# Optimization experiments

Measured on AMD Instinct MI355X. Metric: run time of the kernel, lower is better.

The kernel has to match this reference:

```python
import jax, jax.numpy as jnp
import numpy as np

B = 32768      # batch of ODE state evaluations
N = 64         # input_size (number of variables / per-node MLPs)
H = 64         # hidden_size
N_DISCRETE = 16  # first 16 variables use straight-through gating
HIDDEN_FLAG = True


def setup_inputs() -> dict:
    key = jax.random.key(0)
    k1, k2, k3 = jax.random.split(key, 3)
    inputs = jax.random.normal(k1, (B, N), jnp.float32)
    # Stacked per-node MLP weights: net_i is Linear(N,H,bias=False) -> ReLU -> Linear(H,1,bias=False)
    W1 = jax.random.normal(k2, (N, H, N), jnp.float32) / np.sqrt(N).astype(np.float32)
    W2 = jax.random.normal(k3, (N, H), jnp.float32) / np.sqrt(H).astype(np.float32)
    adjacency = jnp.ones((N, N), jnp.float32)  # buffer, initialized to ones
    discrete_mask = jnp.arange(N) < N_DISCRETE  # bool [N], from input_type_list
    return {"t": 0, "inputs": inputs, "W1": W1, "W2": W2,
            "adjacency": adjacency, "discrete_mask": discrete_mask}


def reference(t, inputs, W1, W2, adjacency, discrete_mask):
    # Straight-through discrete gating: y_hard - sg(y_soft) + y_soft
    y_soft = jax.nn.sigmoid(inputs)
    st = (inputs > 0).astype(inputs.dtype) - jax.lax.stop_gradient(y_soft) + y_soft
    x = jnp.where(discrete_mask[None, :], st, inputs)  # [B, N]

    # Effective per-node input mask: row i of adjacency; last node additionally
    # filtered to only its own (hidden) feature when hidden_flag is set.
    M = adjacency
    if HIDDEN_FLAG:
        one_hot_last = jnp.zeros((N,), M.dtype).at[-1].set(1.0)
        M = M.at[-1].set(M[-1] * one_hot_last)

    # Masking the input of node i by M[i] is equivalent to masking W1[i]'s input dim.
    W1m = W1 * M[:, None, :]                      # [N, H, N]
    h = jax.nn.relu(jnp.einsum('bn,ihn->bih', x, W1m))  # [B, N, H]
    out = jnp.einsum('bih,ih->bi', h, W2)               # [B, N]
    return out
```

## Files before the change

### kernel.cpp

```cpp
#include <hip/hip_runtime.h>
#include <stdint.h>


typedef __attribute__((ext_vector_type(8))) short short8;
typedef __attribute__((ext_vector_type(4))) float floatx4;

#define NN 64
#define HH 64
#define BB 32768
#define OTW 17
#define X_ELEMS (BB * NN)
#define W1_ELEMS (NN * HH * NN)

__device__ __forceinline__ unsigned short f32_to_bf16_bits(float f) {
    union { float f; unsigned int i; } c; c.f = f;
    unsigned int b = c.i;
    b += 0x7fffu + ((b >> 16) & 1u);
    return (unsigned short)(b >> 16);
}

__device__ __forceinline__ bool sniff_bf16(const void* x) {
    const int lane = threadIdx.x & 63;
    const ushort* xw = (const ushort*)x;
    const ushort a = xw[4 * lane];
    const ushort b = xw[4 * lane + 2];
    const int ea = (a >> 7) & 0xFF, eb = (b >> 7) & 0xFF;
    const int hit = ((ea >= 118 && ea <= 132) ? 1 : 0) + ((eb >= 118 && eb <= 132) ? 1 : 0);
    const unsigned long long m1 = __ballot(hit >= 1);
    const unsigned long long m2 = __ballot(hit >= 2);
    return (__popcll(m1) + __popcll(m2)) >= 64;
}

__global__ __launch_bounds__(256, 4)
void prep_kernel(const void* __restrict__ x, const void* __restrict__ w1,
                 ushort* __restrict__ xo, ushort* __restrict__ w1o)
{
    const bool is_bf16 = sniff_bf16(x);
    const long base = ((long)blockIdx.x * 256 + (long)threadIdx.x) * 8;

    if (base < X_ELEMS) {
        const bool gate = (base & 63) < 16;
        short8 v;
        if (is_bf16) {
            v = *(const short8*)((const ushort*)x + base);
            if (gate) {
                #pragma unroll
                for (int j = 0; j < 8; ++j) {
                    const unsigned short u = (unsigned short)v[j];
                    const bool pos = ((u & 0x8000u) == 0) && ((u & 0x7fffu) != 0);
                    v[j] = pos ? (short)0x3F80 : (short)0;
                }
            }
        } else {
            const float* p = (const float*)x + base;
            const float4 f0 = *(const float4*)(p);
            const float4 f1 = *(const float4*)(p + 4);
            const float vals[8] = {f0.x, f0.y, f0.z, f0.w, f1.x, f1.y, f1.z, f1.w};
            #pragma unroll
            for (int j = 0; j < 8; ++j) {
                if (gate) v[j] = (vals[j] > 0.f) ? (short)0x3F80 : (short)0;
                else      v[j] = (short)f32_to_bf16_bits(vals[j]);
            }
        }
        *(short8*)(xo + base) = v;
    } else {
        const long wb = base - X_ELEMS;
        if (wb < W1_ELEMS) {
            short8 v;
            if (is_bf16) {
                v = *(const short8*)((const ushort*)w1 + wb);
            } else {
                const float* p = (const float*)w1 + wb;
                const float4 f0 = *(const float4*)(p);
                const float4 f1 = *(const float4*)(p + 4);
                const float vals[8] = {f0.x, f0.y, f0.z, f0.w, f1.x, f1.y, f1.z, f1.w};
                #pragma unroll
                for (int j = 0; j < 8; ++j) v[j] = (short)f32_to_bf16_bits(vals[j]);
            }
            const int node = (int)(wb >> 12);
            if (node == NN - 1) {
                const int w63 = (int)(wb & 63);
                #pragma unroll
                for (int j = 0; j < 8; ++j)
                    if (w63 + j != NN - 1) v[j] = 0;
            }
            *(short8*)(w1o + wb) = v;
        }
    }
}

template<bool F32>
__device__ __forceinline__ void main_body(const ushort* __restrict__ xo,
                                          const ushort* __restrict__ w1o,
                                          const void* __restrict__ w2p,
                                          void* __restrict__ outp,
                                          float* outTile)
{
    const int tid  = threadIdx.x;
    const int wave = tid >> 6;
    const int lane = tid & 63;
    const int quad = lane >> 4;
    const int l16  = lane & 15;

    const int blk  = blockIdx.x;
    const int ng   = blk >> 9;
    const int rbg  = blk & 511;
    const int b0   = rbg * 64;
    const int nbase = ng * 16 + wave * 4;

    short8 xfrag[2][4];
    #pragma unroll
    for (int ks = 0; ks < 2; ++ks)
        #pragma unroll
        for (int nt = 0; nt < 4; ++nt)
            xfrag[ks][nt] = *(const short8*)(xo + (b0 + nt * 16 + l16) * NN + ks * 32 + quad * 8);

    short8 wcur[2][4], wnxt[2][4];
    {
        const ushort* w1n = w1o + nbase * (HH * NN);
        #pragma unroll
        for (int ks = 0; ks < 2; ++ks)
            #pragma unroll
            for (int mt = 0; mt < 4; ++mt)
                wcur[ks][mt] = *(const short8*)(w1n + (mt * 16 + l16) * NN + ks * 32 + quad * 8);
    }

    #pragma unroll 1
    for (int nl = 0; nl < 4; ++nl) {
        const int node = nbase + nl;

        if (nl < 3) {
            const ushort* w1n = w1o + (node + 1) * (HH * NN);
            #pragma unroll
            for (int ks = 0; ks < 2; ++ks)
                #pragma unroll
                for (int mt = 0; mt < 4; ++mt)
                    wnxt[ks][mt] = *(const short8*)(w1n + (mt * 16 + l16) * NN + ks * 32 + quad * 8);
        }

        float w2v[4][4];
        #pragma unroll
        for (int mt = 0; mt < 4; ++mt) {
            const int idx = node * HH + mt * 16 + quad * 4;
            if (F32) {
                const float4 w = *(const float4*)((const float*)w2p + idx);
                w2v[mt][0] = w.x; w2v[mt][1] = w.y; w2v[mt][2] = w.z; w2v[mt][3] = w.w;
            } else {
                const ushort4 w = *(const ushort4*)((const ushort*)w2p + idx);
                union { unsigned int i; float f; } c0, c1, c2, c3;
                c0.i = ((unsigned int)w.x) << 16; c1.i = ((unsigned int)w.y) << 16;
                c2.i = ((unsigned int)w.z) << 16; c3.i = ((unsigned int)w.w) << 16;
                w2v[mt][0] = c0.f; w2v[mt][1] = c1.f; w2v[mt][2] = c2.f; w2v[mt][3] = c3.f;
            }
        }

        floatx4 acc[4][4];
        #pragma unroll
        for (int mt = 0; mt < 4; ++mt)
            #pragma unroll
            for (int nt = 0; nt < 4; ++nt)
                acc[mt][nt] = (floatx4){0.f, 0.f, 0.f, 0.f};

        #pragma unroll
        for (int ks = 0; ks < 2; ++ks)
            #pragma unroll
            for (int mt = 0; mt < 4; ++mt)
                #pragma unroll
                for (int nt = 0; nt < 4; ++nt)
                    acc[mt][nt] = __builtin_amdgcn_mfma_f32_16x16x32_bf16(
                        wcur[ks][mt], xfrag[ks][nt], acc[mt][nt], 0, 0, 0);

        float psum[4];
        #pragma unroll
        for (int nt = 0; nt < 4; ++nt) {
            float s0 = 0.f, s1 = 0.f;
            #pragma unroll
            for (int mt = 0; mt < 4; ++mt) {
                float a0 = acc[mt][nt][0]; a0 = a0 > 0.f ? a0 : 0.f;
                float a1 = acc[mt][nt][1]; a1 = a1 > 0.f ? a1 : 0.f;
                float a2 = acc[mt][nt][2]; a2 = a2 > 0.f ? a2 : 0.f;
                float a3 = acc[mt][nt][3]; a3 = a3 > 0.f ? a3 : 0.f;
                s0 = fmaf(a0, w2v[mt][0], s0); s1 = fmaf(a1, w2v[mt][1], s1);
                s0 = fmaf(a2, w2v[mt][2], s0); s1 = fmaf(a3, w2v[mt][3], s1);
            }
            psum[nt] = s0 + s1;
        }

        #pragma unroll
        for (int nt = 0; nt < 4; ++nt) {
            psum[nt] += __shfl_xor(psum[nt], 16, 64);
            psum[nt] += __shfl_xor(psum[nt], 32, 64);
        }

        const float val = (quad == 0) ? psum[0] : (quad == 1) ? psum[1]
                         : (quad == 2) ? psum[2] : psum[3];
        outTile[lane * OTW + wave * 4 + nl] = val;

        if (nl < 3) {
            #pragma unroll
            for (int ks = 0; ks < 2; ++ks)
                #pragma unroll
                for (int mt = 0; mt < 4; ++mt)
                    wcur[ks][mt] = wnxt[ks][mt];
        }
    }

    __syncthreads();

    const int row = tid >> 2;
    const int c   = tid & 3;
    const float* rp = outTile + row * OTW + c * 4;
    const float4 v = make_float4(rp[0], rp[1], rp[2], rp[3]);
    const size_t obase = (size_t)(b0 + row) * NN + ng * 16 + c * 4;
    if (F32) {
        *(float4*)((float*)outp + obase) = v;
    } else {
        ushort4 o;
        o.x = f32_to_bf16_bits(v.x); o.y = f32_to_bf16_bits(v.y);
        o.z = f32_to_bf16_bits(v.z); o.w = f32_to_bf16_bits(v.w);
        *(ushort4*)((ushort*)outp + obase) = o;
    }
}

__global__ __launch_bounds__(256, 2)
void main_kernel(const void* __restrict__ xorig,
                 const ushort* __restrict__ xo, const ushort* __restrict__ w1o,
                 const void* __restrict__ w2p, void* __restrict__ outp)
{
    __shared__ float outTile[64 * OTW];
    const bool is_bf16 = sniff_bf16(xorig);
    if (is_bf16) main_body<false>(xo, w1o, w2p, outp, outTile);
    else         main_body<true >(xo, w1o, w2p, outp, outTile);
}

#define LDSW 20
template<bool F32>
__device__ __forceinline__ void run_body_fb(const void* xp, const void* w1p,
                                            const void* w2p, void* outp,
                                            float* myLds)
{
    const int tid  = threadIdx.x;
    const int wave = tid >> 6;
    const int lane = tid & 63;
    const int quad = lane >> 4;
    const int l16  = lane & 15;
    const int blk  = blockIdx.x;
    const int ng   = blk >> 7;
    const int rbg  = blk & 127;
    const int node = ng * 4 + wave;
    const int rowbase = rbg * 256;

    short8 bfrag[2][4];
    #pragma unroll
    for (int ks = 0; ks < 2; ++ks) {
        #pragma unroll
        for (int ht = 0; ht < 4; ++ht) {
            const int h = ht * 16 + l16;
            const int k = ks * 32 + quad * 8;
            short8 v;
            if (F32) {
                const float* p = (const float*)w1p + node * (HH * NN) + h * NN + k;
                const float4 a0 = *(const float4*)(p);
                const float4 a1 = *(const float4*)(p + 4);
                const float vals[8] = {a0.x, a0.y, a0.z, a0.w, a1.x, a1.y, a1.z, a1.w};
                #pragma unroll
                for (int j = 0; j < 8; ++j) v[j] = (short)f32_to_bf16_bits(vals[j]);
            } else {
                v = *(const short8*)((const ushort*)w1p + node * (HH * NN) + h * NN + k);
            }
            if (node == NN - 1) {
                #pragma unroll
                for (int j = 0; j < 8; ++j)
                    if (k + j != NN - 1) v[j] = 0;
            }
            bfrag[ks][ht] = v;
        }
    }

    float w2reg[4];
    #pragma unroll
    for (int ht = 0; ht < 4; ++ht) {
        const int idx = node * HH + ht * 16 + l16;
        if (F32) {
            w2reg[ht] = ((const float*)w2p)[idx];
        } else {
            const ushort u = ((const ushort*)w2p)[idx];
            union { unsigned int i; float f; } cv; cv.i = ((unsigned int)u) << 16;
            w2reg[ht] = cv.f;
        }
    }

    #pragma unroll 1
    for (int it = 0; it < 4; ++it) {
        const int b0 = rowbase + it * 64;
        short8 afrag[2][4];
        #pragma unroll
        for (int ks = 0; ks < 2; ++ks) {
            #pragma unroll
            for (int rt = 0; rt < 4; ++rt) {
                const int rowg = b0 + rt * 16 + l16;
                const int k    = ks * 32 + quad * 8;
                const bool gate = (ks == 0 && quad < 2);
                short8 v;
                if (F32) {
                    const float* p = (const float*)xp + rowg * NN + k;
                    const float4 a0 = *(const float4*)(p);
                    const float4 a1 = *(const float4*)(p + 4);
                    const float vals[8] = {a0.x, a0.y, a0.z, a0.w, a1.x, a1.y, a1.z, a1.w};
                    #pragma unroll
                    for (int j = 0; j < 8; ++j) {
                        if (gate) v[j] = (vals[j] > 0.f) ? (short)0x3F80 : (short)0;
                        else      v[j] = (short)f32_to_bf16_bits(vals[j]);
                    }
                } else {
                    v = *(const short8*)((const ushort*)xp + rowg * NN + k);
                    if (gate) {
                        #pragma unroll
                        for (int j = 0; j < 8; ++j) {
                            const unsigned short u = (unsigned short)v[j];
                            const bool pos = ((u & 0x8000u) == 0) && ((u & 0x7fffu) != 0);
                            v[j] = pos ? (short)0x3F80 : (short)0;
                        }
                    }
                }
                afrag[ks][rt] = v;
            }
        }

        floatx4 acc[4][4];
        #pragma unroll
        for (int rt = 0; rt < 4; ++rt)
            #pragma unroll
            for (int ht = 0; ht < 4; ++ht)
                acc[rt][ht] = (floatx4){0.f, 0.f, 0.f, 0.f};
        #pragma unroll
        for (int ks = 0; ks < 2; ++ks)
            #pragma unroll
            for (int rt = 0; rt < 4; ++rt)
                #pragma unroll
                for (int ht = 0; ht < 4; ++ht)
                    acc[rt][ht] = __builtin_amdgcn_mfma_f32_16x16x32_bf16(
                        afrag[ks][rt], bfrag[ks][ht], acc[rt][ht], 0, 0, 0);

        #pragma unroll
        for (int rt = 0; rt < 4; ++rt) {
            #pragma unroll
            for (int r = 0; r < 4; ++r) {
                float s = 0.f;
                #pragma unroll
                for (int ht = 0; ht < 4; ++ht) {
                    float v = acc[rt][ht][r];
                    v = v > 0.f ? v : 0.f;
                    s = fmaf(v, w2reg[ht], s);
                }
                myLds[(rt * 16 + quad * 4 + r) * LDSW + l16] = s;
            }
        }
        __syncthreads();
        const float* rowp = myLds + lane * LDSW;
        const float4 v0 = *(const float4*)(rowp + 0);
        const float4 v1 = *(const float4*)(rowp + 4);
        const float4 v2 = *(const float4*)(rowp + 8);
        const float4 v3 = *(const float4*)(rowp + 12);
        const float tot = (((v0.x + v0.y) + (v0.z + v0.w)) + ((v1.x + v1.y) + (v1.z + v1.w)))
                        + (((v2.x + v2.y) + (v2.z + v2.w)) + ((v3.x + v3.y) + (v3.z + v3.w)));
        if (F32) ((float*) outp)[(size_t)(b0 + lane) * NN + node] = tot;
        else     ((ushort*)outp)[(size_t)(b0 + lane) * NN + node] = f32_to_bf16_bits(tot);
        __syncthreads();
    }
}

__global__ __launch_bounds__(256, 2)
void fallback_kernel(const void* __restrict__ x, const void* __restrict__ W1,
                     const void* __restrict__ W2, void* __restrict__ out)
{
    __shared__ float lds[4][64 * LDSW];
    const bool is_bf16 = sniff_bf16(x);
    float* myLds = &lds[threadIdx.x >> 6][0];
    if (is_bf16) run_body_fb<false>(x, W1, W2, out, myLds);
    else         run_body_fb<true >(x, W1, W2, out, myLds);
}

extern "C" void kernel_launch(void* const* d_in, const int* in_sizes, int n_in,
                              void* d_out, int out_size, void* d_ws, size_t ws_size,
                              hipStream_t stream) {
    int i_in = -1, i_w1 = -1, i_w2 = -1;
    for (int i = 0; i < n_in; ++i) {
        const int s = in_sizes[i];
        if      (s == BB * NN  && i_in < 0) i_in = i;
        else if (s == NN*HH*NN && i_w1 < 0) i_w1 = i;
        else if (s == NN*HH    && i_w2 < 0) i_w2 = i;
    }
    if (i_in < 0) i_in = (n_in > 1) ? 1 : 0;
    if (i_w1 < 0) i_w1 = i_in + 1;
    if (i_w2 < 0) i_w2 = i_w1 + 1;

    const size_t need = (size_t)(X_ELEMS + W1_ELEMS) * sizeof(ushort);
    if (ws_size >= need) {
        ushort* xo  = (ushort*)d_ws;
        ushort* w1o = xo + X_ELEMS;
        prep_kernel<<<dim3((X_ELEMS + W1_ELEMS) / (256 * 8)), dim3(256), 0, stream>>>(
            d_in[i_in], d_in[i_w1], xo, w1o);
        main_kernel<<<dim3(4 * 512), dim3(256), 0, stream>>>(
            d_in[i_in], xo, w1o, d_in[i_w2], d_out);
    } else {
        fallback_kernel<<<dim3(16 * 128), dim3(256), 0, stream>>>(
            d_in[i_in], d_in[i_w1], d_in[i_w2], d_out);
    }
}
```

Measured before the change: 118.7 us.

## Process all 64 nodes per block to reuse x fragments across nodes

Each block now covers a 64-row batch tile across all 64 nodes, with every wave handling 16 nodes, instead of 16 nodes per block in a grid four times larger. This loads each x tile once instead of four times and writes full 64-wide output rows. W1 double-buffering changes to a ping-pong scheme with two register sets, and the output tile in shared memory widens to 64 columns. The cost is a grid of only 512 blocks, which may underfill the GPU's CUs, plus longer per-block serial work and the same W1 traffic spread over fewer blocks.

```diff
diff --git a/kernel.cpp b/kernel.cpp
--- a/kernel.cpp
+++ b/kernel.cpp
@@ -8,7 +8,7 @@
 #define NN 64
 #define HH 64
 #define BB 32768
-#define OTW 17
+#define OTW 65
 #define X_ELEMS (BB * NN)
 #define W1_ELEMS (NN * HH * NN)
 
@@ -102,11 +102,9 @@
     const int quad = lane >> 4;
     const int l16  = lane & 15;
 
-    const int blk  = blockIdx.x;
-    const int ng   = blk >> 9;
-    const int rbg  = blk & 511;
-    const int b0   = rbg * 64;
-    const int nbase = ng * 16 + wave * 4;
+    const int blk = blockIdx.x;
+    const int b0  = blk * 64;
+    const int nbase = wave * 16;
 
     short8 xfrag[2][4];
     #pragma unroll
@@ -115,41 +113,28 @@
         for (int nt = 0; nt < 4; ++nt)
             xfrag[ks][nt] = *(const short8*)(xo + (b0 + nt * 16 + l16) * NN + ks * 32 + quad * 8);
 
-    short8 wcur[2][4], wnxt[2][4];
-    {
-        const ushort* w1n = w1o + nbase * (HH * NN);
+    auto loadW1 = [&](short8 w[2][4], int node) {
+        const ushort* w1n = w1o + node * (HH * NN);
         #pragma unroll
         for (int ks = 0; ks < 2; ++ks)
             #pragma unroll
             for (int mt = 0; mt < 4; ++mt)
-                wcur[ks][mt] = *(const short8*)(w1n + (mt * 16 + l16) * NN + ks * 32 + quad * 8);
-    }
-
-    #pragma unroll 1
-    for (int nl = 0; nl < 4; ++nl) {
-        const int node = nbase + nl;
-
-        if (nl < 3) {
-            const ushort* w1n = w1o + (node + 1) * (HH * NN);
-            #pragma unroll
-            for (int ks = 0; ks < 2; ++ks)
-                #pragma unroll
-                for (int mt = 0; mt < 4; ++mt)
-                    wnxt[ks][mt] = *(const short8*)(w1n + (mt * 16 + l16) * NN + ks * 32 + quad * 8);
-        }
-
+                w[ks][mt] = *(const short8*)(w1n + (mt * 16 + l16) * NN + ks * 32 + quad * 8);
+    };
+
+    auto computeNode = [&](const short8 w[2][4], int node) {
         float w2v[4][4];
         #pragma unroll
         for (int mt = 0; mt < 4; ++mt) {
             const int idx = node * HH + mt * 16 + quad * 4;
             if (F32) {
-                const float4 w = *(const float4*)((const float*)w2p + idx);
-                w2v[mt][0] = w.x; w2v[mt][1] = w.y; w2v[mt][2] = w.z; w2v[mt][3] = w.w;
+                const float4 ww = *(const float4*)((const float*)w2p + idx);
+                w2v[mt][0] = ww.x; w2v[mt][1] = ww.y; w2v[mt][2] = ww.z; w2v[mt][3] = ww.w;
             } else {
-                const ushort4 w = *(const ushort4*)((const ushort*)w2p + idx);
+                const ushort4 ww = *(const ushort4*)((const ushort*)w2p + idx);
                 union { unsigned int i; float f; } c0, c1, c2, c3;
-                c0.i = ((unsigned int)w.x) << 16; c1.i = ((unsigned int)w.y) << 16;
-                c2.i = ((unsigned int)w.z) << 16; c3.i = ((unsigned int)w.w) << 16;
+                c0.i = ((unsigned int)ww.x) << 16; c1.i = ((unsigned int)ww.y) << 16;
+                c2.i = ((unsigned int)ww.z) << 16; c3.i = ((unsigned int)ww.w) << 16;
                 w2v[mt][0] = c0.f; w2v[mt][1] = c1.f; w2v[mt][2] = c2.f; w2v[mt][3] = c3.f;
             }
         }
@@ -168,7 +153,7 @@
                 #pragma unroll
                 for (int nt = 0; nt < 4; ++nt)
                     acc[mt][nt] = __builtin_amdgcn_mfma_f32_16x16x32_bf16(
-                        wcur[ks][mt], xfrag[ks][nt], acc[mt][nt], 0, 0, 0);
+                        w[ks][mt], xfrag[ks][nt], acc[mt][nt], 0, 0, 0);
 
         float psum[4];
         #pragma unroll
@@ -194,31 +179,41 @@
 
         const float val = (quad == 0) ? psum[0] : (quad == 1) ? psum[1]
                          : (quad == 2) ? psum[2] : psum[3];
-        outTile[lane * OTW + wave * 4 + nl] = val;
-
-        if (nl < 3) {
-            #pragma unroll
-            for (int ks = 0; ks < 2; ++ks)
-                #pragma unroll
-                for (int mt = 0; mt < 4; ++mt)
-                    wcur[ks][mt] = wnxt[ks][mt];
-        }
+        outTile[lane * OTW + node] = val;
+    };
+
+    short8 wA[2][4], wB[2][4];
+    loadW1(wA, nbase);
+    #pragma unroll 1
+    for (int np = 0; np < 16; np += 2) {
+        loadW1(wB, nbase + np + 1);
+        computeNode(wA, nbase + np);
+        if (np + 2 < 16) loadW1(wA, nbase + np + 2);
+        computeNode(wB, nbase + np + 1);
     }
 
     __syncthreads();
 
     const int row = tid >> 2;
-    const int c   = tid & 3;
-    const float* rp = outTile + row * OTW + c * 4;
-    const float4 v = make_float4(rp[0], rp[1], rp[2], rp[3]);
-    const size_t obase = (size_t)(b0 + row) * NN + ng * 16 + c * 4;
+    const int q   = tid & 3;
+    const float* rp = outTile + row * OTW + q * 16;
+    const size_t obase = (size_t)(b0 + row) * NN + q * 16;
     if (F32) {
-        *(float4*)((float*)outp + obase) = v;
+        float* op = (float*)outp + obase;
+        #pragma unroll
+        for (int c = 0; c < 4; ++c) {
+            const float4 v = make_float4(rp[c*4+0], rp[c*4+1], rp[c*4+2], rp[c*4+3]);
+            *(float4*)(op + c * 4) = v;
+        }
     } else {
-        ushort4 o;
-        o.x = f32_to_bf16_bits(v.x); o.y = f32_to_bf16_bits(v.y);
-        o.z = f32_to_bf16_bits(v.z); o.w = f32_to_bf16_bits(v.w);
-        *(ushort4*)((ushort*)outp + obase) = o;
+        ushort* op = (ushort*)outp + obase;
+        #pragma unroll
+        for (int c = 0; c < 4; ++c) {
+            ushort4 o;
+            o.x = f32_to_bf16_bits(rp[c*4+0]); o.y = f32_to_bf16_bits(rp[c*4+1]);
+            o.z = f32_to_bf16_bits(rp[c*4+2]); o.w = f32_to_bf16_bits(rp[c*4+3]);
+            *(ushort4*)(op + c * 4) = o;
+        }
     }
 }
 
@@ -401,7 +396,7 @@
         ushort* w1o = xo + X_ELEMS;
         prep_kernel<<<dim3((X_ELEMS + W1_ELEMS) / (256 * 8)), dim3(256), 0, stream>>>(
             d_in[i_in], d_in[i_w1], xo, w1o);
-        main_kernel<<<dim3(4 * 512), dim3(256), 0, stream>>>(
+        main_kernel<<<dim3(512), dim3(256), 0, stream>>>(
             d_in[i_in], xo, w1o, d_in[i_w2], d_out);
     } else {
         fallback_kernel<<<dim3(16 * 128), dim3(256), 0, stream>>>(
```

New measurement: 115.1 us. -3.0%, faster.

## Retile main kernel to 32 rows by 32 nodes per block with single weight buffer

Applied to the files above, without the earlier changes.

Each block now covers 32 batch rows and 32 nodes (8 nodes per wave) instead of 64 rows and 16 nodes. The double-buffered weight registers become one buffer, with the next node's W1 load issued right after the MFMAs. Launch bounds rise to 3 blocks per SM. The aim is lower register pressure and higher occupancy. The cost is that each W1 fragment is reused over half as many batch rows, so per-wave arithmetic intensity drops and W1 is reloaded more often.

```diff
diff --git a/kernel.cpp b/kernel.cpp
--- a/kernel.cpp
+++ b/kernel.cpp
@@ -8,7 +8,7 @@
 #define NN 64
 #define HH 64
 #define BB 32768
-#define OTW 17
+#define OTW 33
 #define X_ELEMS (BB * NN)
 #define W1_ELEMS (NN * HH * NN)
 
@@ -102,63 +102,54 @@
     const int quad = lane >> 4;
     const int l16  = lane & 15;
 
-    const int blk  = blockIdx.x;
-    const int ng   = blk >> 9;
-    const int rbg  = blk & 511;
-    const int b0   = rbg * 64;
-    const int nbase = ng * 16 + wave * 4;
-
-    short8 xfrag[2][4];
+    const int blk    = blockIdx.x;
+    const int ngrp   = blk >> 10;
+    const int rchunk = blk & 1023;
+    const int b0     = rchunk * 32;
+    const int nbase  = ngrp * 32 + wave * 8;
+
+    short8 xfrag[2][2];
     #pragma unroll
     for (int ks = 0; ks < 2; ++ks)
         #pragma unroll
-        for (int nt = 0; nt < 4; ++nt)
+        for (int nt = 0; nt < 2; ++nt)
             xfrag[ks][nt] = *(const short8*)(xo + (b0 + nt * 16 + l16) * NN + ks * 32 + quad * 8);
 
-    short8 wcur[2][4], wnxt[2][4];
+    short8 w[2][4];
     {
         const ushort* w1n = w1o + nbase * (HH * NN);
         #pragma unroll
         for (int ks = 0; ks < 2; ++ks)
             #pragma unroll
             for (int mt = 0; mt < 4; ++mt)
-                wcur[ks][mt] = *(const short8*)(w1n + (mt * 16 + l16) * NN + ks * 32 + quad * 8);
+                w[ks][mt] = *(const short8*)(w1n + (mt * 16 + l16) * NN + ks * 32 + quad * 8);
     }
 
     #pragma unroll 1
-    for (int nl = 0; nl < 4; ++nl) {
+    for (int nl = 0; nl < 8; ++nl) {
         const int node = nbase + nl;
-
-        if (nl < 3) {
-            const ushort* w1n = w1o + (node + 1) * (HH * NN);
-            #pragma unroll
-            for (int ks = 0; ks < 2; ++ks)
-                #pragma unroll
-                for (int mt = 0; mt < 4; ++mt)
-                    wnxt[ks][mt] = *(const short8*)(w1n + (mt * 16 + l16) * NN + ks * 32 + quad * 8);
-        }
 
         float w2v[4][4];
         #pragma unroll
         for (int mt = 0; mt < 4; ++mt) {
             const int idx = node * HH + mt * 16 + quad * 4;
             if (F32) {
-                const float4 w = *(const float4*)((const float*)w2p + idx);
-                w2v[mt][0] = w.x; w2v[mt][1] = w.y; w2v[mt][2] = w.z; w2v[mt][3] = w.w;
+                const float4 ww = *(const float4*)((const float*)w2p + idx);
+                w2v[mt][0] = ww.x; w2v[mt][1] = ww.y; w2v[mt][2] = ww.z; w2v[mt][3] = ww.w;
             } else {
-                const ushort4 w = *(const ushort4*)((const ushort*)w2p + idx);
+                const ushort4 ww = *(const ushort4*)((const ushort*)w2p + idx);
                 union { unsigned int i; float f; } c0, c1, c2, c3;
-                c0.i = ((unsigned int)w.x) << 16; c1.i = ((unsigned int)w.y) << 16;
-                c2.i = ((unsigned int)w.z) << 16; c3.i = ((unsigned int)w.w) << 16;
+                c0.i = ((unsigned int)ww.x) << 16; c1.i = ((unsigned int)ww.y) << 16;
+                c2.i = ((unsigned int)ww.z) << 16; c3.i = ((unsigned int)ww.w) << 16;
                 w2v[mt][0] = c0.f; w2v[mt][1] = c1.f; w2v[mt][2] = c2.f; w2v[mt][3] = c3.f;
             }
         }
 
-        floatx4 acc[4][4];
+        floatx4 acc[4][2];
         #pragma unroll
         for (int mt = 0; mt < 4; ++mt)
             #pragma unroll
-            for (int nt = 0; nt < 4; ++nt)
+            for (int nt = 0; nt < 2; ++nt)
                 acc[mt][nt] = (floatx4){0.f, 0.f, 0.f, 0.f};
 
         #pragma unroll
@@ -166,13 +157,22 @@
             #pragma unroll
             for (int mt = 0; mt < 4; ++mt)
                 #pragma unroll
-                for (int nt = 0; nt < 4; ++nt)
+                for (int nt = 0; nt < 2; ++nt)
                     acc[mt][nt] = __builtin_amdgcn_mfma_f32_16x16x32_bf16(
-                        wcur[ks][mt], xfrag[ks][nt], acc[mt][nt], 0, 0, 0);
-
-        float psum[4];
-        #pragma unroll
-        for (int nt = 0; nt < 4; ++nt) {
+                        w[ks][mt], xfrag[ks][nt], acc[mt][nt], 0, 0, 0);
+
+        if (nl < 7) {
+            const ushort* w1n = w1o + (node + 1) * (HH * NN);
+            #pragma unroll
+            for (int ks = 0; ks < 2; ++ks)
+                #pragma unroll
+                for (int mt = 0; mt < 4; ++mt)
+                    w[ks][mt] = *(const short8*)(w1n + (mt * 16 + l16) * NN + ks * 32 + quad * 8);
+        }
+
+        float psum[2];
+        #pragma unroll
+        for (int nt = 0; nt < 2; ++nt) {
             float s0 = 0.f, s1 = 0.f;
             #pragma unroll
             for (int mt = 0; mt < 4; ++mt) {
@@ -187,47 +187,40 @@
         }
 
         #pragma unroll
-        for (int nt = 0; nt < 4; ++nt) {
+        for (int nt = 0; nt < 2; ++nt) {
             psum[nt] += __shfl_xor(psum[nt], 16, 64);
             psum[nt] += __shfl_xor(psum[nt], 32, 64);
         }
 
-        const float val = (quad == 0) ? psum[0] : (quad == 1) ? psum[1]
-                         : (quad == 2) ? psum[2] : psum[3];
-        outTile[lane * OTW + wave * 4 + nl] = val;
-
-        if (nl < 3) {
-            #pragma unroll
-            for (int ks = 0; ks < 2; ++ks)
-                #pragma unroll
-                for (int mt = 0; mt < 4; ++mt)
-                    wcur[ks][mt] = wnxt[ks][mt];
-        }
+        const int half = lane >> 5;
+        const float val = half ? psum[1] : psum[0];
+        if ((lane & 16) == 0)
+            outTile[(half * 16 + l16) * OTW + wave * 8 + nl] = val;
     }
 
     __syncthreads();
 
-    const int row = tid >> 2;
-    const int c   = tid & 3;
+    const int row = tid >> 3;
+    const int c   = tid & 7;
     const float* rp = outTile + row * OTW + c * 4;
-    const float4 v = make_float4(rp[0], rp[1], rp[2], rp[3]);
-    const size_t obase = (size_t)(b0 + row) * NN + ng * 16 + c * 4;
+    const size_t obase = (size_t)(b0 + row) * NN + ngrp * 32 + c * 4;
     if (F32) {
+        const float4 v = make_float4(rp[0], rp[1], rp[2], rp[3]);
         *(float4*)((float*)outp + obase) = v;
     } else {
         ushort4 o;
-        o.x = f32_to_bf16_bits(v.x); o.y = f32_to_bf16_bits(v.y);
-        o.z = f32_to_bf16_bits(v.z); o.w = f32_to_bf16_bits(v.w);
+        o.x = f32_to_bf16_bits(rp[0]); o.y = f32_to_bf16_bits(rp[1]);
+        o.z = f32_to_bf16_bits(rp[2]); o.w = f32_to_bf16_bits(rp[3]);
         *(ushort4*)((ushort*)outp + obase) = o;
     }
 }
 
-__global__ __launch_bounds__(256, 2)
+__global__ __launch_bounds__(256, 3)
 void main_kernel(const void* __restrict__ xorig,
                  const ushort* __restrict__ xo, const ushort* __restrict__ w1o,
                  const void* __restrict__ w2p, void* __restrict__ outp)
 {
-    __shared__ float outTile[64 * OTW];
+    __shared__ float outTile[32 * OTW];
     const bool is_bf16 = sniff_bf16(xorig);
     if (is_bf16) main_body<false>(xo, w1o, w2p, outp, outTile);
     else         main_body<true >(xo, w1o, w2p, outp, outTile);
@@ -401,7 +394,7 @@
         ushort* w1o = xo + X_ELEMS;
         prep_kernel<<<dim3((X_ELEMS + W1_ELEMS) / (256 * 8)), dim3(256), 0, stream>>>(
             d_in[i_in], d_in[i_w1], xo, w1o);
-        main_kernel<<<dim3(4 * 512), dim3(256), 0, stream>>>(
+        main_kernel<<<dim3(2 * 1024), dim3(256), 0, stream>>>(
             d_in[i_in], xo, w1o, d_in[i_w2], d_out);
     } else {
         fallback_kernel<<<dim3(16 * 128), dim3(256), 0, stream>>>(
```

Measured after the change: 142.2 us. +19.8%, slower.
